# Performance work log

Measured on AMD Instinct MI355X. Metric: run time of the kernel, lower is better.

Reference implementation:

```python
import jax, jax.numpy as jnp
import numpy as np

K = 4
KS = 7
SHIFT = KS // 2

def setup_inputs() -> dict:
    key = jax.random.key(0)
    ks = jax.random.split(key, 5)
    B, C, H, W = 8, 128, 256, 256
    x = jax.random.normal(ks[0], (B, C, H, W), dtype=jnp.float32)
    guidance = jax.random.normal(ks[1], (B, C, H, W), dtype=jnp.float32)
    basis_filters = jax.random.normal(ks[2], (K, C, KS, KS), dtype=jnp.float32)
    w1 = jax.random.normal(ks[3], (C // 4, C), dtype=jnp.float32) * (1.0 / np.sqrt(C))
    b1 = jnp.zeros((C // 4,), dtype=jnp.float32)
    w2 = jax.random.normal(ks[4], (K, C // 4), dtype=jnp.float32) * (1.0 / np.sqrt(C // 4))
    b2 = jnp.zeros((K,), dtype=jnp.float32)
    return {"x": x, "guidance": guidance, "basis_filters": basis_filters,
            "w1": w1, "b1": b1, "w2": w2, "b2": b2}

def reference(x, guidance, basis_filters, w1, b1, w2, b2):
    B, C, H, W = x.shape
    # guidance vector: global average pool -> MLP -> softmax over k bases
    g = jnp.mean(guidance, axis=(2, 3))                      # [B, C]
    h1 = jax.nn.relu(g @ w1.T + b1)                          # [B, C//4]
    weights = jax.nn.softmax(h1 @ w2.T + b2, axis=1)         # [B, K]
    # dynamic per-sample depthwise kernel: weighted sum of bases
    dyn = jnp.einsum('bk,kcij->bcij', weights, basis_filters)  # [B, C, KS, KS]
    # pad kernel to full (H, W) at the bottom/right, then roll to center at origin
    padded = jnp.pad(dyn, ((0, 0), (0, 0), (0, H - KS), (0, W - KS)))
    centered = jnp.roll(padded, shift=(-SHIFT, -SHIFT), axis=(-2, -1))
    # circular depthwise convolution via FFT
    filt_fft = jnp.fft.rfft2(centered, s=(H, W), axes=(-2, -1))
    x_fft = jnp.fft.rfft2(x, s=(H, W), axes=(-2, -1))
    out = jnp.fft.irfft2(x_fft * filt_fft, s=(H, W), axes=(-2, -1))
    return out
```

## Files before the change

### kernel.cpp

```cpp
#include <hip/hip_runtime.h>

#define HW 256
#define HWMASK 255
#define CH 128
#define BATCH 8
#define NK 4
#define TSY 16
#define QR 66
#define RRING 40
#define NT 8

typedef float f32x4 __attribute__((ext_vector_type(4)));

__device__ __forceinline__ void load_lds16(const void* g, void* l) {
    __builtin_amdgcn_global_load_lds((const __attribute__((address_space(1))) void*)g,
                                     (__attribute__((address_space(3))) void*)l, 16, 0, 0);
}

__device__ __forceinline__ void stage_rows(const float* xp, float4* ring,
                                           int row0, int nrows, int tid) {
    int slot0 = ((row0 % RRING) + RRING) % RRING;
    int total = nrows * QR;
    float4* base = ring + slot0 * QR;
    #pragma unroll 1
    for (int off = 0; off < total; off += 256) {
        int e = off + tid;
        if (e < total) {
            int ro = e / QR, q = e - ro * QR;
            int gy = (row0 + ro) & HWMASK;
            int gx = (4 * q - 4) & HWMASK;
            load_lds16(xp + gy * HW + gx, &base[e]);
        }
    }
}

__global__ __launch_bounds__(256) void mean1_kernel(const float* __restrict__ guid,
                                                    float* __restrict__ partial) {
    int blk = blockIdx.x;
    const float4* p = (const float4*)(guid + (size_t)blk * 16384);
    float s = 0.f;
    for (int i = threadIdx.x; i < 4096; i += 256) {
        float4 v = p[i];
        s += (v.x + v.y) + (v.z + v.w);
    }
    for (int off = 32; off; off >>= 1) s += __shfl_down(s, off, 64);
    __shared__ float red[4];
    if ((threadIdx.x & 63) == 0) red[threadIdx.x >> 6] = s;
    __syncthreads();
    if (threadIdx.x == 0) partial[blk] = (red[0] + red[1]) + (red[2] + red[3]);
}

__global__ __launch_bounds__(256) void mlp_kernel(const float* __restrict__ partial,
                                                  const float* __restrict__ w1,
                                                  const float* __restrict__ b1,
                                                  const float* __restrict__ w2,
                                                  const float* __restrict__ b2,
                                                  float* __restrict__ wt) {
    __shared__ float gs[BATCH * CH];
    __shared__ float h1[BATCH * 32];
    __shared__ float lg[BATCH * NK];
    int t = threadIdx.x;
    for (int i = t; i < BATCH * CH; i += 256) {
        float4 v = *(const float4*)(partial + i * 4);
        gs[i] = ((v.x + v.y) + (v.z + v.w)) * (1.0f / 65536.0f);
    }
    __syncthreads();
    {
        int b = t >> 5, j = t & 31;
        float acc = b1[j];
        #pragma unroll 4
        for (int c = 0; c < CH; ++c) acc += gs[b * CH + c] * w1[j * CH + c];
        h1[b * 32 + j] = fmaxf(acc, 0.f);
    }
    __syncthreads();
    if (t < BATCH * NK) {
        int b = t >> 2, k = t & 3;
        float acc = b2[k];
        #pragma unroll
        for (int j = 0; j < 32; ++j) acc += h1[b * 32 + j] * w2[k * 32 + j];
        lg[b * NK + k] = acc;
    }
    __syncthreads();
    if (t < BATCH) {
        int b = t;
        float m = lg[b * 4];
        for (int k = 1; k < 4; ++k) m = fmaxf(m, lg[b * 4 + k]);
        float e[4], s = 0.f;
        for (int k = 0; k < 4; ++k) { e[k] = expf(lg[b * 4 + k] - m); s += e[k]; }
        float inv = 1.0f / s;
        for (int k = 0; k < 4; ++k) wt[b * 4 + k] = e[k] * inv;
    }
}

__global__ __launch_bounds__(256) void dyn_kernel(const float* __restrict__ wt,
                                                  const float* __restrict__ basis,
                                                  float* __restrict__ dynF) {
    int idx = blockIdx.x * 256 + threadIdx.x;
    if (idx >= BATCH * CH * 49) return;
    int ij = idx % 49;
    int bc = idx / 49;
    int c = bc % CH;
    int b = bc / CH;
    float acc = 0.f;
    #pragma unroll
    for (int k = 0; k < NK; ++k)
        acc += wt[b * NK + k] * basis[(k * CH + c) * 49 + ij];
    dynF[bc * 49 + (48 - ij)] = acc;
}

__global__ __launch_bounds__(256) void conv_kernel(const float* __restrict__ x,
                                                   const float* __restrict__ dynF,
                                                   float* __restrict__ out) {
    int bc = blockIdx.x;
    int ybase = blockIdx.y * (NT * TSY);
    __shared__ float4 ring[RRING * QR];
    const float* xp = x + (size_t)bc * (HW * HW);
    float* op = out + (size_t)bc * (HW * HW);
    int tid = threadIdx.x;

    const float* df = dynF + bc * 49;
    float d[49];
    #pragma unroll
    for (int i = 0; i < 49; ++i) d[i] = df[i];

    {
        int row0 = ybase - 3;
        int s0 = ((row0 % RRING) + RRING) % RRING;
        int p1 = min(22, RRING - s0);
        stage_rows(xp, ring, row0, p1, tid);
        if (p1 < 22) stage_rows(xp, ring, row0 + p1, 22 - p1, tid);
    }
    asm volatile("s_waitcnt vmcnt(0)" ::: "memory");
    __builtin_amdgcn_s_barrier();

    int tx = tid & 63, ty = tid >> 6;
    int ly0 = 4 * ty;

    #pragma unroll 1
    for (int t = 0; t < NT; ++t) {
        if (t + 1 < NT) {
            int rb = ybase + 16 * t + 19;
            int s0 = rb % RRING;
            int p1 = min(16, RRING - s0);
            stage_rows(xp, ring, rb, p1, tid);
            if (p1 < 16) stage_rows(xp, ring, rb + p1, 16 - p1, tid);
        }

        int y0 = ybase + 16 * t + ly0;
        float acc[4][4] = {};
        #pragma unroll
        for (int rr = 0; rr < 10; ++rr) {
            int row = y0 + rr - 3;
            int slot = ((row % RRING) + RRING) % RRING;
            const float4* rp = &ring[slot * QR + tx];
            float4 A = rp[0], B = rp[1], C = rp[2];
            float v[12] = {A.x, A.y, A.z, A.w, B.x, B.y, B.z, B.w, C.x, C.y, C.z, C.w};
            #pragma unroll
            for (int rq = 0; rq < 4; ++rq) {
                int ii = rr - rq;
                if (ii >= 0 && ii <= 6) {
                    #pragma unroll
                    for (int q = 0; q < 4; ++q) {
                        #pragma unroll
                        for (int jj = 0; jj < 7; ++jj)
                            acc[rq][q] += d[ii * 7 + jj] * v[q + jj + 1];
                    }
                }
            }
        }
        #pragma unroll
        for (int rq = 0; rq < 4; ++rq) {
            f32x4 o = {acc[rq][0], acc[rq][1], acc[rq][2], acc[rq][3]};
            __builtin_nontemporal_store(o, (f32x4*)(op + (y0 + rq) * HW + 4 * tx));
        }

        if (t + 1 < NT) {
            asm volatile("s_waitcnt vmcnt(4)" ::: "memory");
            __builtin_amdgcn_s_barrier();
        }
    }
}

extern "C" void kernel_launch(void* const* d_in, const int* in_sizes, int n_in,
                              void* d_out, int out_size, void* d_ws, size_t ws_size,
                              hipStream_t stream) {
    const float* x        = (const float*)d_in[0];
    const float* guidance = (const float*)d_in[1];
    const float* basis    = (const float*)d_in[2];
    const float* w1       = (const float*)d_in[3];
    const float* b1       = (const float*)d_in[4];
    const float* w2       = (const float*)d_in[5];
    const float* b2       = (const float*)d_in[6];
    float* out = (float*)d_out;
    float* ws  = (float*)d_ws;

    float* partial = ws;
    float* wt      = ws + 4096;
    float* dynF    = ws + 4096 + 32;

    mean1_kernel<<<4096, 256, 0, stream>>>(guidance, partial);
    mlp_kernel<<<1, 256, 0, stream>>>(partial, w1, b1, w2, b2, wt);
    dyn_kernel<<<(BATCH * CH * 49 + 255) / 256, 256, 0, stream>>>(wt, basis, dynF);
    conv_kernel<<<dim3(BATCH * CH, HW / (NT * TSY)), 256, 0, stream>>>(x, dynF, out);
}
```

Before: 199.4 us.

## Replace async global-to-LDS staging with register prefetch and ring writes

Drops the global_load_lds DMA path. Each thread now prefetches the next 16-row tile into registers before computing the current tile, then writes those registers into a 38-row LDS ring after the compute and before a barrier. Ring slot indexing is simplified to incremental pointers, replacing the per-row modulo arithmetic, and the per-thread row and column offsets are precomputed once. This costs extra VGPRs for the five float4 prefetch buffers and adds explicit ds_write instructions on every tile.

```diff
diff --git a/kernel.cpp b/kernel.cpp
--- a/kernel.cpp
+++ b/kernel.cpp
@@ -7,32 +7,10 @@
 #define NK 4
 #define TSY 16
 #define QR 66
-#define RRING 40
+#define RING 38
 #define NT 8
 
 typedef float f32x4 __attribute__((ext_vector_type(4)));
-
-__device__ __forceinline__ void load_lds16(const void* g, void* l) {
-    __builtin_amdgcn_global_load_lds((const __attribute__((address_space(1))) void*)g,
-                                     (__attribute__((address_space(3))) void*)l, 16, 0, 0);
-}
-
-__device__ __forceinline__ void stage_rows(const float* xp, float4* ring,
-                                           int row0, int nrows, int tid) {
-    int slot0 = ((row0 % RRING) + RRING) % RRING;
-    int total = nrows * QR;
-    float4* base = ring + slot0 * QR;
-    #pragma unroll 1
-    for (int off = 0; off < total; off += 256) {
-        int e = off + tid;
-        if (e < total) {
-            int ro = e / QR, q = e - ro * QR;
-            int gy = (row0 + ro) & HWMASK;
-            int gx = (4 * q - 4) & HWMASK;
-            load_lds16(xp + gy * HW + gx, &base[e]);
-        }
-    }
-}
 
 __global__ __launch_bounds__(256) void mean1_kernel(const float* __restrict__ guid,
                                                     float* __restrict__ partial) {
@@ -113,7 +91,7 @@
                                                    float* __restrict__ out) {
     int bc = blockIdx.x;
     int ybase = blockIdx.y * (NT * TSY);
-    __shared__ float4 ring[RRING * QR];
+    __shared__ float4 ring[RING * QR];
     const float* xp = x + (size_t)bc * (HW * HW);
     float* op = out + (size_t)bc * (HW * HW);
     int tid = threadIdx.x;
@@ -124,35 +102,57 @@
     for (int i = 0; i < 49; ++i) d[i] = df[i];
 
     {
-        int row0 = ybase - 3;
-        int s0 = ((row0 % RRING) + RRING) % RRING;
-        int p1 = min(22, RRING - s0);
-        stage_rows(xp, ring, row0, p1, tid);
-        if (p1 < 22) stage_rows(xp, ring, row0 + p1, 22 - p1, tid);
-    }
-    asm volatile("s_waitcnt vmcnt(0)" ::: "memory");
-    __builtin_amdgcn_s_barrier();
+        int s0 = (ybase - 3 + RING * 8) % RING;
+        const int PE[6] = {0, 256, 512, 768, 1024, 1196};
+        #pragma unroll
+        for (int k = 0; k < 6; ++k) {
+            int e = PE[k] + tid;
+            int ro = e / QR, q = e - ro * QR;
+            int gy = (ybase - 3 + ro) & HWMASK;
+            int gx = (4 * q - 4) & HWMASK;
+            int s = s0 + ro; if (s >= RING) s -= RING;
+            ring[s * QR + q] = *(const float4*)(xp + gy * HW + gx);
+        }
+    }
+    __syncthreads();
+
+    int r0, r1, r2, r3, r4;
+    int q0, q1, q2, q3, q4;
+    int x0, x1, x2, x3, x4;
+    {
+        int e;
+        e = tid;       r0 = e / QR; q0 = e - r0 * QR; x0 = (4 * q0 - 4) & HWMASK;
+        e = 256 + tid; r1 = e / QR; q1 = e - r1 * QR; x1 = (4 * q1 - 4) & HWMASK;
+        e = 512 + tid; r2 = e / QR; q2 = e - r2 * QR; x2 = (4 * q2 - 4) & HWMASK;
+        e = 768 + tid; r3 = e / QR; q3 = e - r3 * QR; x3 = (4 * q3 - 4) & HWMASK;
+        e = 800 + tid; r4 = e / QR; q4 = e - r4 * QR; x4 = (4 * q4 - 4) & HWMASK;
+    }
 
     int tx = tid & 63, ty = tid >> 6;
     int ly0 = 4 * ty;
+    int sb  = (ybase - 3 + RING * 8) % RING;
+    int rbm = (ybase + 19) % RING;
+
+    float4 pf0, pf1, pf2, pf3, pf4;
 
     #pragma unroll 1
     for (int t = 0; t < NT; ++t) {
         if (t + 1 < NT) {
             int rb = ybase + 16 * t + 19;
-            int s0 = rb % RRING;
-            int p1 = min(16, RRING - s0);
-            stage_rows(xp, ring, rb, p1, tid);
-            if (p1 < 16) stage_rows(xp, ring, rb + p1, 16 - p1, tid);
+            int gy;
+            gy = (rb + r0) & HWMASK; pf0 = *(const float4*)(xp + gy * HW + x0);
+            gy = (rb + r1) & HWMASK; pf1 = *(const float4*)(xp + gy * HW + x1);
+            gy = (rb + r2) & HWMASK; pf2 = *(const float4*)(xp + gy * HW + x2);
+            gy = (rb + r3) & HWMASK; pf3 = *(const float4*)(xp + gy * HW + x3);
+            gy = (rb + r4) & HWMASK; pf4 = *(const float4*)(xp + gy * HW + x4);
         }
 
         int y0 = ybase + 16 * t + ly0;
         float acc[4][4] = {};
         #pragma unroll
         for (int rr = 0; rr < 10; ++rr) {
-            int row = y0 + rr - 3;
-            int slot = ((row % RRING) + RRING) % RRING;
-            const float4* rp = &ring[slot * QR + tx];
+            int s = sb + ly0 + rr; if (s >= RING) s -= RING;
+            const float4* rp = &ring[s * QR + tx];
             float4 A = rp[0], B = rp[1], C = rp[2];
             float v[12] = {A.x, A.y, A.z, A.w, B.x, B.y, B.z, B.w, C.x, C.y, C.z, C.w};
             #pragma unroll
@@ -175,9 +175,17 @@
         }
 
         if (t + 1 < NT) {
-            asm volatile("s_waitcnt vmcnt(4)" ::: "memory");
+            int s;
+            s = rbm + r0; if (s >= RING) s -= RING; ring[s * QR + q0] = pf0;
+            s = rbm + r1; if (s >= RING) s -= RING; ring[s * QR + q1] = pf1;
+            s = rbm + r2; if (s >= RING) s -= RING; ring[s * QR + q2] = pf2;
+            s = rbm + r3; if (s >= RING) s -= RING; ring[s * QR + q3] = pf3;
+            s = rbm + r4; if (s >= RING) s -= RING; ring[s * QR + q4] = pf4;
+            asm volatile("s_waitcnt lgkmcnt(0)" ::: "memory");
             __builtin_amdgcn_s_barrier();
         }
+        sb += 16;  if (sb  >= RING) sb  -= RING;
+        rbm += 16; if (rbm >= RING) rbm -= RING;
     }
 }
 
```

New measurement: 188.2 us. 5.6% less time.
